# Optimization experiments

Hardware: AMD Instinct MI355X
Metric: run time of the kernel (lower is better)

Reference implementation:

```python
import jax, jax.numpy as jnp
import numpy as np

NEG_INF = -1e9
LRELU_SLOPE = 0.2  # torch GAT default leaky_relu negative slope


def setup_inputs() -> dict:
    key = jax.random.key(0)
    k1, k2, k3, k4, k5 = jax.random.split(key, 5)
    N, F_IN, H, DH = 4096, 1433, 8, 8  # n_nodes, in_features, n_heads, per-head dim (n_hidden=64)
    vert = jax.random.normal(k1, (N, F_IN), dtype=jnp.float32)
    edge = jax.random.randint(k2, (N, N), 0, 2, dtype=jnp.int32)  # dense adjacency mask
    W = jax.random.normal(k3, (F_IN, H * DH), dtype=jnp.float32) * 0.05
    a_l = jax.random.normal(k4, (H, DH), dtype=jnp.float32) * 0.05
    a_r = jax.random.normal(k5, (H, DH), dtype=jnp.float32) * 0.05
    return {"vert": vert, "edge": edge, "W": W, "a_l": a_l, "a_r": a_r}


def reference(vert, edge, W, a_l, a_r):
    # GAT-style edge-affinity layer (is_concat=True) + ELU; dropout is identity (eval mode).
    N = vert.shape[0]
    H, DH = a_l.shape
    g = (vert @ W).reshape(N, H, DH)                      # [N,H,Dh] projected node features
    sl = jnp.einsum('nhd,hd->nh', g, a_l)                 # source-node attention term
    sr = jnp.einsum('nhd,hd->nh', g, a_r)                 # target-node attention term
    e = sl[:, None, :] + sr[None, :, :]                   # [N,N,H]: attn([g_i || g_j])
    e = jnp.where(e >= 0, e, LRELU_SLOPE * e)             # leaky_relu
    mask = (edge != 0)[:, :, None]                        # [N,N,1]
    e = jnp.where(mask, e, NEG_INF)                       # mask non-edges
    a = jax.nn.softmax(e, axis=1)                         # normalize over neighbors j
    out = jnp.einsum('ijh,jhd->ihd', a, g).reshape(N, H * DH)  # aggregate + concat heads
    return jax.nn.elu(out)
```

## Files before the change

kernel.cpp:

```cpp
#include <hip/hip_runtime.h>
#include <hip/hip_bf16.h>

#define NN 4096
#define FIN 1433
#define NH 8
#define DH 8
#define HD 64
#define KP 1472
#define LOG2E 1.44269504f
#define NJS 4
#define NCHK ((NN / NJS) / 128)

typedef unsigned int u32;
typedef unsigned long long u64;
typedef float v4f __attribute__((ext_vector_type(4)));
typedef _Float16 f16;
typedef _Float16 h2 __attribute__((ext_vector_type(2)));
typedef _Float16 f16x8 __attribute__((ext_vector_type(8)));

static __device__ __forceinline__ short f2h16(float f) {
    union { f16 h; short s; } u; u.h = (f16)f; return u.s;
}
static __device__ __forceinline__ h2 u2h2(u32 x) {
    union { u32 u; h2 h; } v; v.u = x; return v.h;
}
static __device__ __forceinline__ u32 h22u(h2 x) {
    union { h2 h; u32 u; } v; v.h = x; return v.u;
}

#if __has_builtin(__builtin_amdgcn_sbfe)
#define SBFE1(x, k) __builtin_amdgcn_sbfe((int)(x), (k), 1)
#else
#define SBFE1(x, k) (((int)((x) << (31 - (k)))) >> 31)
#endif

__global__ __launch_bounds__(256) void k_eprep(const int* __restrict__ edge,
                                               uint4* __restrict__ emask) {
    const int t = threadIdx.x, lane = t & 63, w = t >> 6;
    const int row = blockIdx.x;
    const int* erow = edge + (size_t)row * NN;
    uint4* mrow = emask + (size_t)row * (NN / 128);
#pragma unroll
    for (int it = 0; it < 8; ++it) {
        const int ck = w * 8 + it;
        const int2 e2 = *(const int2*)&erow[ck * 128 + 2 * lane];
        const u64 bA = __ballot(e2.x != 0);
        const u64 bB = __ballot(e2.y != 0);
        if (lane == 0)
            mrow[ck] = (uint4){(u32)bA, (u32)(bA >> 32), (u32)bB, (u32)(bB >> 32)};
    }
}

__global__ __launch_bounds__(256) void k_wprep(const float* __restrict__ W,
                                               short* __restrict__ Wt) {
    __shared__ float Ts[64][65];
    const int c = blockIdx.x;
    const int u = threadIdx.x;
    const int n4 = (u & 15) * 4;
    const int kr = u >> 4;
#pragma unroll
    for (int q = 0; q < 4; ++q) {
        const int kl = kr + q * 16;
        const int kg = c * 64 + kl;
        v4f v = {0.f, 0.f, 0.f, 0.f};
        if (kg < FIN) v = *(const v4f*)&W[(size_t)kg * HD + n4];
        *(v4f*)&Ts[kl][n4] = v;
    }
    __syncthreads();
    const int n = u >> 2;
    const int koff = (u & 3) * 16;
    __align__(16) short tmp[16];
#pragma unroll
    for (int r = 0; r < 16; ++r) tmp[r] = f2h16(Ts[koff + r][n]);
    *(uint4*)&Wt[(size_t)n * KP + c * 64 + koff]     = *(uint4*)&tmp[0];
    *(uint4*)&Wt[(size_t)n * KP + c * 64 + koff + 8] = *(uint4*)&tmp[8];
}

__global__ __launch_bounds__(256, 4) void k_gemm(
    const float* __restrict__ vert, const short* __restrict__ Wt,
    const float* __restrict__ al, const float* __restrict__ ar,
    short* __restrict__ gT, short* __restrict__ eB, short* __restrict__ eD,
    float* __restrict__ Rw)
{
    __shared__ float cacc[4][16][64];

    const int t = threadIdx.x, lane = t & 63, w = t >> 6;
    const int ml = lane & 15, q = lane >> 4;
    const int i0 = blockIdx.x * 16;
    const float* vrow = vert + (size_t)(i0 + ml) * FIN;

    v4f acc[4];
#pragma unroll
    for (int g = 0; g < 4; ++g) acc[g] = (v4f){0.f, 0.f, 0.f, 0.f};

    for (int c = w; c < 45; c += 4) {
        const int k0 = c * 32 + q * 8;
        v4f a0, a1;
        if (k0 + 7 < FIN) {
            a0 = *(const v4f*)&vrow[k0];
            a1 = *(const v4f*)&vrow[k0 + 4];
        } else {
            float tmp[8];
#pragma unroll
            for (int e = 0; e < 8; ++e)
                tmp[e] = (k0 + e < FIN) ? vrow[k0 + e] : 0.f;
            a0 = (v4f){tmp[0], tmp[1], tmp[2], tmp[3]};
            a1 = (v4f){tmp[4], tmp[5], tmp[6], tmp[7]};
        }
        const f16x8 af = {(f16)a0.x, (f16)a0.y, (f16)a0.z, (f16)a0.w,
                          (f16)a1.x, (f16)a1.y, (f16)a1.z, (f16)a1.w};
#pragma unroll
        for (int g = 0; g < 4; ++g) {
            const f16x8 bf = *(const f16x8*)&Wt[(size_t)(g * 16 + ml) * KP + k0];
            acc[g] = __builtin_amdgcn_mfma_f32_16x16x32_f16(af, bf, acc[g], 0, 0, 0);
        }
    }

#pragma unroll
    for (int g = 0; g < 4; ++g)
#pragma unroll
        for (int r = 0; r < 4; ++r)
            cacc[w][q * 4 + r][g * 16 + ml] = acc[g][r];
    __syncthreads();

    const int m = t >> 4, n4 = (t & 15) * 4;
    v4f s = (v4f){0.f, 0.f, 0.f, 0.f};
#pragma unroll
    for (int ww = 0; ww < 4; ++ww) s += *(const v4f*)&cacc[ww][m][n4];

#pragma unroll
    for (int e = 0; e < 4; ++e)
        gT[(size_t)(n4 + e) * NN + i0 + m] = f2h16(s[e]);

    float pl = s.x * al[n4] + s.y * al[n4 + 1] + s.z * al[n4 + 2] + s.w * al[n4 + 3];
    float pr = s.x * ar[n4] + s.y * ar[n4 + 1] + s.z * ar[n4 + 2] + s.w * ar[n4 + 3];
    pl += __shfl_xor(pl, 1, 64);
    pr += __shfl_xor(pr, 1, 64);
    if ((t & 1) == 0) {
        const int h = (t & 15) >> 1;
        const int node = i0 + m;
        eB[h * NN + node] = f2h16(exp2f(pr * LOG2E));
        eD[h * NN + node] = f2h16(exp2f(0.2f * pr * LOG2E));
        Rw[node * NH + h] = exp2f(-0.8f * pl * LOG2E);
    }
}

__global__ __launch_bounds__(256, 4) void k_attn(
    const uint4* __restrict__ emask, const short* __restrict__ gT,
    const short* __restrict__ eB, const short* __restrict__ eD,
    const float* __restrict__ Rw,
    float* __restrict__ numw, float* __restrict__ denw)
{
    __shared__ __align__(16) short Gt[2][64][136];

    const int t = threadIdx.x, lane = t & 63, w = t >> 6;
    const int ml = lane & 15, quad = lane >> 4;
    const int m8 = ml & 7;
    const int i0 = blockIdx.x * 16;
    const int js = blockIdx.y;
    const int jbase = js * (NN / NJS);
    const int h0 = w, h1 = w + 4;
    const int qb4 = quad * 4;
    const bool mhi = (ml >= 8);
    const u32 one2 = 0x3C003C00u;
    const uint4 ones4 = (uint4){one2, one2, one2, one2};

    h2 Ri[2];
    {
        const f16 r0 = (f16)Rw[(i0 + ml) * NH + h0];
        const f16 r1 = (f16)Rw[(i0 + ml) * NH + h1];
        Ri[0] = (h2){r0, r0};
        Ri[1] = (h2){r1, r1};
    }

    const uint4* mrow = emask + (size_t)(i0 + ml) * (NN / 128) + js * NCHK;
    const short* bp0 = eB + (size_t)h0 * NN + jbase;
    const short* dp0 = eD + (size_t)h0 * NN + jbase;
    const short* bp1 = eB + (size_t)h1 * NN + jbase;
    const short* dp1 = eD + (size_t)h1 * NN + jbase;

    const int grow = t >> 3, gseg = (t & 7) * 16;
    const short* g0 = gT + (size_t)grow * NN + jbase;
    const short* g1 = gT + (size_t)(grow + 32) * NN + jbase;

    {
        *(uint4*)&Gt[0][grow][gseg]          = *(const uint4*)&g0[gseg];
        *(uint4*)&Gt[0][grow][gseg + 8]      = *(const uint4*)&g0[gseg + 8];
        *(uint4*)&Gt[0][grow + 32][gseg]     = *(const uint4*)&g1[gseg];
        *(uint4*)&Gt[0][grow + 32][gseg + 8] = *(const uint4*)&g1[gseg + 8];
    }
    uint4 mw = mrow[0];
    __syncthreads();

    v4f acc[2];
    acc[0] = (v4f){0.f, 0.f, 0.f, 0.f};
    acc[1] = (v4f){0.f, 0.f, 0.f, 0.f};

    for (int c = 0; c < NCHK; ++c) {
        const int cb = c & 1, nb = cb ^ 1;
        const bool pf = (c + 1) < NCHK;
        uint4 pg0, pg1, pg2, pg3, pm;
        if (pf) {
            const int jn = (c + 1) * 128;
            pg0 = *(const uint4*)&g0[jn + gseg];
            pg1 = *(const uint4*)&g0[jn + gseg + 8];
            pg2 = *(const uint4*)&g1[jn + gseg];
            pg3 = *(const uint4*)&g1[jn + gseg + 8];
            pm  = mrow[c + 1];
        }
#pragma unroll
        for (int s = 0; s < 4; ++s) {
            const int j0 = c * 128 + s * 32 + quad * 8;
            const uint4 bu0 = *(const uint4*)&bp0[j0];
            const uint4 du0 = *(const uint4*)&dp0[j0];
            const uint4 bu1 = *(const uint4*)&bp1[j0];
            const uint4 du1 = *(const uint4*)&dp1[j0];
            const uint4 gu0 = *(const uint4*)&Gt[cb][h0 * 8 + m8][s * 32 + quad * 8];
            const uint4 gu1 = *(const uint4*)&Gt[cb][h1 * 8 + m8][s * 32 + quad * 8];
            const int base = ((s & 1) << 4) + qb4;
            const u32 WA = ((s >> 1) ? mw.y : mw.x) >> base;
            const u32 WB = ((s >> 1) ? mw.w : mw.z) >> base;
            u32 m[4];
#pragma unroll
            for (int k = 0; k < 4; ++k) {
                const int ea = SBFE1(WA, k);
                const int eb = SBFE1(WB, k);
                m[k] = __builtin_amdgcn_perm((u32)eb, (u32)ea, 0x05040100u);
            }
            u32 aw0[4], aw1[4];
#pragma unroll
            for (int k = 0; k < 4; ++k) {
                const u32 rd0 = h22u(Ri[0] * u2h2((&du0.x)[k]));
                const u32 rd1 = h22u(Ri[1] * u2h2((&du1.x)[k]));
                u32 p0, p1;
                asm("v_pk_max_f16 %0, %1, %2" : "=v"(p0) : "v"(rd0), "v"((&bu0.x)[k]));
                asm("v_pk_max_f16 %0, %1, %2" : "=v"(p1) : "v"(rd1), "v"((&bu1.x)[k]));
                aw0[k] = p0 & m[k];
                aw1[k] = p1 & m[k];
            }
            union { uint4 u; f16x8 h; } a0u, a1u, g0u, g1u;
            a0u.u = (uint4){aw0[0], aw0[1], aw0[2], aw0[3]};
            a1u.u = (uint4){aw1[0], aw1[1], aw1[2], aw1[3]};
            g0u.u = mhi ? ones4 : gu0;
            g1u.u = mhi ? ones4 : gu1;
            acc[0] = __builtin_amdgcn_mfma_f32_16x16x32_f16(a0u.h, g0u.h, acc[0], 0, 0, 0);
            acc[1] = __builtin_amdgcn_mfma_f32_16x16x32_f16(a1u.h, g1u.h, acc[1], 0, 0, 0);
        }
        if (pf) {
            *(uint4*)&Gt[nb][grow][gseg]          = pg0;
            *(uint4*)&Gt[nb][grow][gseg + 8]      = pg1;
            *(uint4*)&Gt[nb][grow + 32][gseg]     = pg2;
            *(uint4*)&Gt[nb][grow + 32][gseg + 8] = pg3;
            mw = pm;
        }
        __syncthreads();
    }

    float* nw = numw + (size_t)js * NN * HD;
    float* dw = denw + (size_t)js * NN * NH;
    const int ibase = i0 + quad * 4;
#pragma unroll
    for (int hh = 0; hh < 2; ++hh) {
        const int h = w + hh * 4;
#pragma unroll
        for (int r = 0; r < 4; ++r) {
            if (ml < 8)       nw[(ibase + r) * HD + h * 8 + ml] = acc[hh][r];
            else if (ml == 8) dw[(ibase + r) * NH + h]          = acc[hh][r];
        }
    }
}

__global__ __launch_bounds__(256) void k_comb(
    const float* __restrict__ numw, const float* __restrict__ denw,
    float* __restrict__ out)
{
    const int gid = blockIdx.x * 256 + threadIdx.x;
    const int i = gid >> 6, h = (gid & 63) >> 3;
    float num = 0.f, den = 0.f;
#pragma unroll
    for (int s = 0; s < NJS; ++s) {
        num += numw[s * NN * HD + gid];
        den += denw[s * NN * NH + i * NH + h];
    }
    float x = num / den;
    out[gid] = (x > 0.f) ? x : (__expf(x) - 1.f);
}

extern "C" void kernel_launch(void* const* d_in, const int* in_sizes, int n_in,
                              void* d_out, int out_size, void* d_ws, size_t ws_size,
                              hipStream_t stream) {
    const float* vert = (const float*)d_in[0];
    const int*   edge = (const int*)d_in[1];
    const float* W    = (const float*)d_in[2];
    const float* al   = (const float*)d_in[3];
    const float* ar   = (const float*)d_in[4];
    float* out = (float*)d_out;

    char* ws = (char*)d_ws;
    short* gT    = (short*)ws;
    short* eB    = (short*)(ws + 512 * 1024);
    short* eD    = (short*)(ws + 576 * 1024);
    float* Rw    = (float*)(ws + 640 * 1024);
    short* Wt    = (short*)(ws + 768 * 1024);
    uint4* emask = (uint4*)(ws + 1024 * 1024);
    float* numw  = (float*)(ws + 3 * 1024 * 1024);
    float* denw  = (float*)(ws + 7 * 1024 * 1024);

    hipLaunchKernelGGL(k_eprep, dim3(NN), dim3(256), 0, stream, edge, emask);
    hipLaunchKernelGGL(k_wprep, dim3(23), dim3(256), 0, stream, W, Wt);
    hipLaunchKernelGGL(k_gemm, dim3(NN / 16), dim3(256), 0, stream,
                       vert, Wt, al, ar, gT, eB, eD, Rw);
    hipLaunchKernelGGL(k_attn, dim3(NN / 16, NJS), dim3(256), 0, stream,
                       emask, gT, eB, eD, Rw, numw, denw);
    hipLaunchKernelGGL(k_comb, dim3(NN * HD / 256), dim3(256), 0, stream,
                       numw, denw, out);
}
```

Baseline: 170.2 us.

## Split GEMM over K with a separate reduce kernel and widen the attention j-split

The projection GEMM is split into four K-slices across a second grid dimension, each writing fp32 partial results. A new k_gpost kernel sums the partials and computes the attention exponent terms. The attention kernel's j-dimension split grows from 4 to 8, its shared buffer goes from double to single with an extra barrier per chunk, and its launch bound targets 8 blocks per SM. The aim is more parallelism for the GEMM (256 blocks previously) and higher occupancy in attention, paid for by an extra launch, partial-sum traffic, and a larger combine workload.

```diff
diff --git a/kernel.cpp b/kernel.cpp
--- a/kernel.cpp
+++ b/kernel.cpp
@@ -8,8 +8,9 @@
 #define HD 64
 #define KP 1472
 #define LOG2E 1.44269504f
-#define NJS 4
+#define NJS 8
 #define NCHK ((NN / NJS) / 128)
+#define NKS 4
 
 typedef unsigned int u32;
 typedef unsigned long long u64;
@@ -78,22 +79,21 @@
 
 __global__ __launch_bounds__(256, 4) void k_gemm(
     const float* __restrict__ vert, const short* __restrict__ Wt,
-    const float* __restrict__ al, const float* __restrict__ ar,
-    short* __restrict__ gT, short* __restrict__ eB, short* __restrict__ eD,
-    float* __restrict__ Rw)
+    float* __restrict__ Cp)
 {
-    __shared__ float cacc[4][16][64];
+    __shared__ float cacc[4][16][68];
 
     const int t = threadIdx.x, lane = t & 63, w = t >> 6;
     const int ml = lane & 15, q = lane >> 4;
     const int i0 = blockIdx.x * 16;
+    const int ks = blockIdx.y;
     const float* vrow = vert + (size_t)(i0 + ml) * FIN;
 
     v4f acc[4];
 #pragma unroll
     for (int g = 0; g < 4; ++g) acc[g] = (v4f){0.f, 0.f, 0.f, 0.f};
 
-    for (int c = w; c < 45; c += 4) {
+    for (int c = ks + 4 * w; c < 45; c += 16) {
         const int k0 = c * 32 + q * 8;
         v4f a0, a1;
         if (k0 + 7 < FIN) {
@@ -127,10 +127,27 @@
     v4f s = (v4f){0.f, 0.f, 0.f, 0.f};
 #pragma unroll
     for (int ww = 0; ww < 4; ++ww) s += *(const v4f*)&cacc[ww][m][n4];
+    *(v4f*)&Cp[((size_t)ks * NN + i0 + m) * HD + n4] = s;
+}
+
+__global__ __launch_bounds__(256) void k_gpost(
+    const float* __restrict__ Cp,
+    const float* __restrict__ al, const float* __restrict__ ar,
+    short* __restrict__ gT, short* __restrict__ eB, short* __restrict__ eD,
+    float* __restrict__ Rw)
+{
+    const int t = threadIdx.x;
+    const int gid = blockIdx.x * 256 + t;
+    const int i = gid >> 4, n4 = (gid & 15) * 4;
+
+    v4f s = (v4f){0.f, 0.f, 0.f, 0.f};
+#pragma unroll
+    for (int ks = 0; ks < NKS; ++ks)
+        s += *(const v4f*)&Cp[((size_t)ks * NN + i) * HD + n4];
 
 #pragma unroll
     for (int e = 0; e < 4; ++e)
-        gT[(size_t)(n4 + e) * NN + i0 + m] = f2h16(s[e]);
+        gT[(size_t)(n4 + e) * NN + i] = f2h16(s[e]);
 
     float pl = s.x * al[n4] + s.y * al[n4 + 1] + s.z * al[n4 + 2] + s.w * al[n4 + 3];
     float pr = s.x * ar[n4] + s.y * ar[n4 + 1] + s.z * ar[n4 + 2] + s.w * ar[n4 + 3];
@@ -138,20 +155,19 @@
     pr += __shfl_xor(pr, 1, 64);
     if ((t & 1) == 0) {
         const int h = (t & 15) >> 1;
-        const int node = i0 + m;
-        eB[h * NN + node] = f2h16(exp2f(pr * LOG2E));
-        eD[h * NN + node] = f2h16(exp2f(0.2f * pr * LOG2E));
-        Rw[node * NH + h] = exp2f(-0.8f * pl * LOG2E);
-    }
-}
-
-__global__ __launch_bounds__(256, 4) void k_attn(
+        eB[h * NN + i] = f2h16(exp2f(pr * LOG2E));
+        eD[h * NN + i] = f2h16(exp2f(0.2f * pr * LOG2E));
+        Rw[i * NH + h] = exp2f(-0.8f * pl * LOG2E);
+    }
+}
+
+__global__ __launch_bounds__(256, 8) void k_attn(
     const uint4* __restrict__ emask, const short* __restrict__ gT,
     const short* __restrict__ eB, const short* __restrict__ eD,
     const float* __restrict__ Rw,
     float* __restrict__ numw, float* __restrict__ denw)
 {
-    __shared__ __align__(16) short Gt[2][64][136];
+    __shared__ __align__(16) short Gt[64][136];
 
     const int t = threadIdx.x, lane = t & 63, w = t >> 6;
     const int ml = lane & 15, quad = lane >> 4;
@@ -183,23 +199,24 @@
     const short* g0 = gT + (size_t)grow * NN + jbase;
     const short* g1 = gT + (size_t)(grow + 32) * NN + jbase;
 
-    {
-        *(uint4*)&Gt[0][grow][gseg]          = *(const uint4*)&g0[gseg];
-        *(uint4*)&Gt[0][grow][gseg + 8]      = *(const uint4*)&g0[gseg + 8];
-        *(uint4*)&Gt[0][grow + 32][gseg]     = *(const uint4*)&g1[gseg];
-        *(uint4*)&Gt[0][grow + 32][gseg + 8] = *(const uint4*)&g1[gseg + 8];
-    }
-    uint4 mw = mrow[0];
-    __syncthreads();
+    uint4 pg0 = *(const uint4*)&g0[gseg];
+    uint4 pg1 = *(const uint4*)&g0[gseg + 8];
+    uint4 pg2 = *(const uint4*)&g1[gseg];
+    uint4 pg3 = *(const uint4*)&g1[gseg + 8];
+    uint4 mw = mrow[0], pm;
 
     v4f acc[2];
     acc[0] = (v4f){0.f, 0.f, 0.f, 0.f};
     acc[1] = (v4f){0.f, 0.f, 0.f, 0.f};
 
     for (int c = 0; c < NCHK; ++c) {
-        const int cb = c & 1, nb = cb ^ 1;
+        __syncthreads();
+        *(uint4*)&Gt[grow][gseg]          = pg0;
+        *(uint4*)&Gt[grow][gseg + 8]      = pg1;
+        *(uint4*)&Gt[grow + 32][gseg]     = pg2;
+        *(uint4*)&Gt[grow + 32][gseg + 8] = pg3;
+        __syncthreads();
         const bool pf = (c + 1) < NCHK;
-        uint4 pg0, pg1, pg2, pg3, pm;
         if (pf) {
             const int jn = (c + 1) * 128;
             pg0 = *(const uint4*)&g0[jn + gseg];
@@ -215,8 +232,8 @@
             const uint4 du0 = *(const uint4*)&dp0[j0];
             const uint4 bu1 = *(const uint4*)&bp1[j0];
             const uint4 du1 = *(const uint4*)&dp1[j0];
-            const uint4 gu0 = *(const uint4*)&Gt[cb][h0 * 8 + m8][s * 32 + quad * 8];
-            const uint4 gu1 = *(const uint4*)&Gt[cb][h1 * 8 + m8][s * 32 + quad * 8];
+            const uint4 gu0 = *(const uint4*)&Gt[h0 * 8 + m8][s * 32 + quad * 8];
+            const uint4 gu1 = *(const uint4*)&Gt[h1 * 8 + m8][s * 32 + quad * 8];
             const int base = ((s & 1) << 4) + qb4;
             const u32 WA = ((s >> 1) ? mw.y : mw.x) >> base;
             const u32 WB = ((s >> 1) ? mw.w : mw.z) >> base;
@@ -246,14 +263,7 @@
             acc[0] = __builtin_amdgcn_mfma_f32_16x16x32_f16(a0u.h, g0u.h, acc[0], 0, 0, 0);
             acc[1] = __builtin_amdgcn_mfma_f32_16x16x32_f16(a1u.h, g1u.h, acc[1], 0, 0, 0);
         }
-        if (pf) {
-            *(uint4*)&Gt[nb][grow][gseg]          = pg0;
-            *(uint4*)&Gt[nb][grow][gseg + 8]      = pg1;
-            *(uint4*)&Gt[nb][grow + 32][gseg]     = pg2;
-            *(uint4*)&Gt[nb][grow + 32][gseg + 8] = pg3;
-            mw = pm;
-        }
-        __syncthreads();
+        if (pf) mw = pm;
     }
 
     float* nw = numw + (size_t)js * NN * HD;
@@ -303,13 +313,16 @@
     float* Rw    = (float*)(ws + 640 * 1024);
     short* Wt    = (short*)(ws + 768 * 1024);
     uint4* emask = (uint4*)(ws + 1024 * 1024);
-    float* numw  = (float*)(ws + 3 * 1024 * 1024);
-    float* denw  = (float*)(ws + 7 * 1024 * 1024);
+    float* Cp    = (float*)(ws + 3 * 1024 * 1024);
+    float* numw  = (float*)(ws + 7 * 1024 * 1024);
+    float* denw  = (float*)(ws + 15 * 1024 * 1024);
 
     hipLaunchKernelGGL(k_eprep, dim3(NN), dim3(256), 0, stream, edge, emask);
     hipLaunchKernelGGL(k_wprep, dim3(23), dim3(256), 0, stream, W, Wt);
-    hipLaunchKernelGGL(k_gemm, dim3(NN / 16), dim3(256), 0, stream,
-                       vert, Wt, al, ar, gT, eB, eD, Rw);
+    hipLaunchKernelGGL(k_gemm, dim3(NN / 16, NKS), dim3(256), 0, stream,
+                       vert, Wt, Cp);
+    hipLaunchKernelGGL(k_gpost, dim3(NN * 16 / 256), dim3(256), 0, stream,
+                       Cp, al, ar, gT, eB, eD, Rw);
     hipLaunchKernelGGL(k_attn, dim3(NN / 16, NJS), dim3(256), 0, stream,
                        emask, gT, eB, eD, Rw, numw, denw);
     hipLaunchKernelGGL(k_comb, dim3(NN * HD / 256), dim3(256), 0, stream,
```

Measured after the change: 161.5 us. 5.1% less time.
